# Performance work log

Measured on AMD Instinct MI355X. Metric: run time of the kernel, lower is better.

## Reference

```python
import jax, jax.numpy as jnp
import numpy as np

ALPHA = 0.2  # LeakyReLU negative slope
MASK_FILL = -9e15


def setup_inputs() -> dict:
    key = jax.random.key(0)
    k_x, k_adj, k_W, k_a = jax.random.split(key, 4)
    B, N, Fin, T, O = 8, 1024, 64, 8, 128
    x = jax.random.normal(k_x, (B, N, Fin, T), dtype=jnp.float32)
    adj = (jax.random.uniform(k_adj, (N, N)) < 0.05).astype(jnp.float32)
    adj = jnp.maximum(adj, jnp.eye(N, dtype=jnp.float32))
    W = jax.random.normal(k_W, (Fin, O), dtype=jnp.float32) * (1.414 * (6.0 / (Fin + O)) ** 0.5)
    a = jax.random.normal(k_a, (2 * O, 1), dtype=jnp.float32) * (1.414 * (6.0 / (2 * O + 1)) ** 0.5)
    return {"x": x, "adj": adj, "W": W, "a": a}


def reference(x, adj, W, a):
    # x: (B, N, Fin, T), adj: (N, N), W: (Fin, O), a: (2O, 1)
    O = W.shape[1]
    xt = jnp.transpose(x, (0, 3, 1, 2))                 # (B, T, N, Fin)
    Wh = jnp.einsum('btnf,fo->btno', xt, W)             # (B, T, N, O)
    a1 = a[:O, 0]                                       # (O,)
    a2 = a[O:, 0]                                       # (O,)
    Wh1 = Wh @ a1                                       # (B, T, N)
    Wh2 = Wh @ a2                                       # (B, T, N)
    e = Wh1[..., :, None] + Wh2[..., None, :]           # (B, T, N, N): e_ij = Wh1_i + Wh2_j
    e = jax.nn.leaky_relu(e, negative_slope=ALPHA)
    e = jnp.where(adj > 0, e, MASK_FILL)
    attn = jax.nn.softmax(e, axis=-1)                   # softmax over neighbors j (torch dim=1 on (N,N))
    # dropout on attention is identity at inference (training=False)
    h_prime = jnp.einsum('btij,btjo->btio', attn, Wh)   # (B, T, N, O)
    out = jnp.transpose(h_prime, (0, 2, 3, 1))          # (B, N, O, T)
    return jax.nn.elu(out)                              # concat=True -> ELU
```

## Files before the change

kernel.cpp:

```cpp
#include <hip/hip_runtime.h>
#include <math.h>
#include <stdint.h>

#define ALPHA 0.2f

typedef __attribute__((ext_vector_type(8)))  short bf16x8;
typedef __attribute__((ext_vector_type(4)))  float f32x4;
typedef __attribute__((ext_vector_type(16))) float f32x16;

__device__ __forceinline__ uint32_t pack_bf16(float a, float b) {
    return ((__float_as_uint(a) + 0x8000u) >> 16) |
           ((__float_as_uint(b) + 0x8000u) & 0xFFFF0000u);
}

__global__ __launch_bounds__(512) void k_wh(const float* __restrict__ x,
                                            const float* __restrict__ W,
                                            const float* __restrict__ a,
                                            uint4* __restrict__ Whf,
                                            float* __restrict__ Wh1,
                                            float* __restrict__ Wh2) {
    __shared__ float xs[16 * 512];
    __shared__ float Wv[128 * 68];

    const int tid = threadIdx.x;
    const int b   = blockIdx.x & 7;
    const int jt  = blockIdx.x >> 3;

    const float4* xg4 = (const float4*)(x + (size_t)(b * 1024 + jt * 16) * 512);
    #pragma unroll
    for (int i = 0; i < 4; ++i) {
        int    idx = tid + i * 512;
        float4 v   = xg4[idx];
        int jl  = idx >> 7;
        int rem = idx & 127;
        int f   = rem >> 1;
        int tq  = rem & 1;
        int kk  = f ^ ((jl >> 2) << 2);
        float* dst = &xs[jl * 512 + (tq * 4) * 64 + kk];
        dst[0]   = v.x;
        dst[64]  = v.y;
        dst[128] = v.z;
        dst[192] = v.w;
    }
    const float4* Wg4 = (const float4*)W;
    #pragma unroll
    for (int i = 0; i < 4; ++i) {
        int    idx = tid + i * 512;
        float4 v   = Wg4[idx];
        int k  = idx >> 5;
        int o0 = (idx & 31) * 4;
        #pragma unroll
        for (int c = 0; c < 4; ++c) {
            int o   = o0 + c;
            int adr = o * 68 + ((((k >> 2) ^ ((o >> 3) & 7)) << 2) | (k & 3));
            Wv[adr] = (&v.x)[c];
        }
    }
    __syncthreads();

    const int w  = tid >> 6;
    const int l  = tid & 63;
    const int q  = l >> 4;
    const int om = l & 15;
    const int t  = w;

    float acc[4][8];
    #pragma unroll
    for (int jj = 0; jj < 4; ++jj)
        #pragma unroll
        for (int nt = 0; nt < 8; ++nt) acc[jj][nt] = 0.f;

    for (int kc = 0; kc < 64; kc += 4) {
        float4 xv[4], wv[8];
        const int kx = kc ^ (q << 2);
        #pragma unroll
        for (int jj = 0; jj < 4; ++jj)
            xv[jj] = *(const float4*)&xs[(q * 4 + jj) * 512 + t * 64 + kx];
        #pragma unroll
        for (int nt = 0; nt < 8; ++nt) {
            int og  = nt * 16 + om;
            int grp = (kc >> 2) ^ ((nt * 2 + (om >> 3)) & 7);
            wv[nt]  = *(const float4*)&Wv[og * 68 + grp * 4];
        }
        #pragma unroll
        for (int jj = 0; jj < 4; ++jj) {
            #pragma unroll
            for (int nt = 0; nt < 8; ++nt) {
                float s = acc[jj][nt];
                s = fmaf(xv[jj].x, wv[nt].x, s);
                s = fmaf(xv[jj].y, wv[nt].y, s);
                s = fmaf(xv[jj].z, wv[nt].z, s);
                s = fmaf(xv[jj].w, wv[nt].w, s);
                acc[jj][nt] = s;
            }
        }
    }

    const int bt = b * 8 + t;

    float a1v[8], a2v[8];
    #pragma unroll
    for (int nt = 0; nt < 8; ++nt) {
        a1v[nt] = a[nt * 16 + om];
        a2v[nt] = a[128 + nt * 16 + om];
    }
    #pragma unroll
    for (int jj = 0; jj < 4; ++jj) {
        float s1 = 0.f, s2 = 0.f;
        #pragma unroll
        for (int nt = 0; nt < 8; ++nt) {
            s1 = fmaf(acc[jj][nt], a1v[nt], s1);
            s2 = fmaf(acc[jj][nt], a2v[nt], s2);
        }
        #pragma unroll
        for (int off = 1; off < 16; off <<= 1) {
            s1 += __shfl_xor(s1, off);
            s2 += __shfl_xor(s2, off);
        }
        if (om == 0) {
            int j = jt * 16 + q * 4 + jj;
            Wh1[bt * 1024 + j] = s1;
            Wh2[bt * 1024 + j] = s2;
        }
    }

    #pragma unroll
    for (int nt = 0; nt < 8; ++nt) {
        uint2 st;
        st.x = pack_bf16(acc[0][nt], acc[1][nt]);
        st.y = pack_bf16(acc[2][nt], acc[3][nt]);
        int    lane2 = ((q >> 1) << 5) | ((nt & 1) << 4) | om;
        size_t fidx  = ((size_t)(bt * 4 + (nt >> 1)) * 64 + jt) * 64 + lane2;
        char*  p     = (char*)(Whf + fidx) + ((q & 1) << 3);
        *(uint2*)p = st;
    }
}

__global__ __launch_bounds__(256) void k_adjb(const float* __restrict__ adj,
                                              unsigned char* __restrict__ adjq) {
    int idx = blockIdx.x * 256 + threadIdx.x;
    int i   = idx >> 7;
    int pos = idx & 127;
    const float4* a4 = (const float4*)adj + idx * 2;
    float4 v0 = a4[0], v1 = a4[1];
    unsigned int by = 0;
    by |= (v0.x > 0.f) ? 1u : 0u;
    by |= (v0.y > 0.f) ? 2u : 0u;
    by |= (v0.z > 0.f) ? 4u : 0u;
    by |= (v0.w > 0.f) ? 8u : 0u;
    by |= (v1.x > 0.f) ? 16u : 0u;
    by |= (v1.y > 0.f) ? 32u : 0u;
    by |= (v1.z > 0.f) ? 64u : 0u;
    by |= (v1.w > 0.f) ? 128u : 0u;
    adjq[(i << 7) + ((pos & 1) << 6) + (((pos >> 1) & 1) << 5) + (pos >> 2)] = (unsigned char)by;
}

__global__ __launch_bounds__(256) void k_agg(const uint4* __restrict__ Whf,
                                             const float* __restrict__ Wh1,
                                             const float* __restrict__ Wh2,
                                             const unsigned char* __restrict__ adjq,
                                             float* __restrict__ out) {
    __shared__ __attribute__((aligned(16))) uint4    bstage[2][1024];
    __shared__ __attribute__((aligned(16))) uint32_t efs[1024];
    __shared__ float wh1s[128];
    __shared__ float m2s[4];

    const int tid   = threadIdx.x;
    const int b     = blockIdx.x & 7;
    const int t     = (blockIdx.x >> 3) & 7;
    const int itile = blockIdx.x >> 6;
    const int bt    = b * 8 + t;
    const int i0    = itile * 128;

    const int w   = tid >> 6;
    const int l   = tid & 63;
    const int col = l & 31;
    const int g   = l >> 5;
    const int row = w * 32 + col;

    const uint4* plane = Whf + (size_t)bt * 16384;
    const int    c     = w;
    const int    li    = l;

    uint4 pf[4];
    #pragma unroll
    for (int f = 0; f < 4; ++f) pf[f] = plane[(c * 64 + f) * 64 + li];

    const uint4* ap = (const uint4*)(adjq + ((size_t)(i0 + row) << 7) + (g << 6));
    uint4 am[4];
    #pragma unroll
    for (int f = 0; f < 4; ++f) am[f] = ap[f];

    const float* wh2g = Wh2 + bt * 1024;
    float mx = -1e30f;
    #pragma unroll
    for (int rep = 0; rep < 4; ++rep) {
        int   j  = tid + rep * 256;
        float h2 = wh2g[j];
        float E  = __expf(h2);
        float F  = __expf(ALPHA * h2);
        efs[j] = pack_bf16(E, F);
        mx = fmaxf(mx, h2);
    }
    #pragma unroll
    for (int off = 1; off < 64; off <<= 1) mx = fmaxf(mx, __shfl_xor(mx, off));
    if (l == 0) m2s[w] = mx;
    if (tid < 128) wh1s[tid] = Wh1[bt * 1024 + i0 + tid];

    #pragma unroll
    for (int f = 0; f < 4; ++f) bstage[0][(c * 4 + f) * 64 + li] = pf[f];
    __syncthreads();

    const float M2 = fmaxf(fmaxf(m2s[0], m2s[1]), fmaxf(m2s[2], m2s[3]));
    const float h1 = wh1s[row];
    const float e0 = h1 + M2;
    const float mp = fmaxf(e0, ALPHA * e0);
    const float Af = __expf(h1 - mp);
    const float Bf = __expf(ALPHA * h1 - mp);
    const float G  = __expf(-h1);

    f32x16 acc[4];
    #pragma unroll
    for (int nt2 = 0; nt2 < 4; ++nt2)
        #pragma unroll
        for (int r = 0; r < 16; ++r) acc[nt2][r] = 0.f;
    f32x16 accl;
    #pragma unroll
    for (int r = 0; r < 16; ++r) accl[r] = 0.f;

    bf16x8 ones;
    #pragma unroll
    for (int i = 0; i < 8; ++i) ones[i] = (short)0x3F80;

    #pragma unroll
    for (int u = 0; u < 16; ++u) {
        if (u + 1 < 16) {
            #pragma unroll
            for (int f = 0; f < 4; ++f)
                pf[f] = plane[(c * 64 + (u + 1) * 4 + f) * 64 + li];
        }

        #pragma unroll
        for (int d = 0; d < 2; ++d) {
            const int s = u * 2 + d;
            #pragma unroll
            for (int h = 0; h < 2; ++h) {
                const int jb = s * 32 + h * 16 + g * 8;
                uint4 efa = *(const uint4*)&efs[jb];
                uint4 efb = *(const uint4*)&efs[jb + 4];
                uint32_t ef[8] = {efa.x, efa.y, efa.z, efa.w,
                                  efb.x, efb.y, efb.z, efb.w};

                const int      pe = h * 32 + s;
                const uint4    av = am[pe >> 4];
                const int      cc = (pe >> 2) & 3;
                const uint32_t cw = (cc == 0) ? av.x : (cc == 1) ? av.y
                                   : (cc == 2) ? av.z : av.w;
                const uint32_t by = (cw >> ((pe & 3) * 8)) & 0xFFu;

                float p[8];
                #pragma unroll
                for (int e = 0; e < 8; ++e) {
                    float E  = __uint_as_float(ef[e] << 16);
                    float F  = __uint_as_float(ef[e] & 0xFFFF0000u);
                    bool  cd = E > G;
                    float pr = (cd ? Af : Bf) * (cd ? E : F);
                    p[e] = ((by >> e) & 1u) ? pr : 0.0f;
                }
                union { uint32_t u32[4]; bf16x8 v; } pk;
                #pragma unroll
                for (int r = 0; r < 4; ++r)
                    pk.u32[r] = pack_bf16(p[2 * r], p[2 * r + 1]);

                #pragma unroll
                for (int nt2 = 0; nt2 < 4; ++nt2) {
                    union { uint4 u4; bf16x8 v; } br;
                    br.u4 = bstage[u & 1][(nt2 * 4 + d * 2 + h) * 64 + l];
                    acc[nt2] = __builtin_amdgcn_mfma_f32_32x32x16_bf16(
                        pk.v, br.v, acc[nt2], 0, 0, 0);
                }
                accl = __builtin_amdgcn_mfma_f32_32x32x16_bf16(
                    pk.v, ones, accl, 0, 0, 0);
            }
        }

        if (u + 1 < 16) {
            #pragma unroll
            for (int f = 0; f < 4; ++f)
                bstage[(u + 1) & 1][(c * 4 + f) * 64 + li] = pf[f];
        }
        __syncthreads();
    }

    float* og = out + ((size_t)(b * 1024 + i0 + w * 32)) * 1024 + t;
    #pragma unroll
    for (int reg = 0; reg < 16; ++reg) {
        const int   r    = (reg & 3) + 8 * (reg >> 2) + 4 * g;
        const float linv = 1.0f / accl[reg];
        #pragma unroll
        for (int nt2 = 0; nt2 < 4; ++nt2) {
            float v = acc[nt2][reg] * linv;
            v = v > 0.f ? v : __expf(v) - 1.f;
            og[(size_t)r * 1024 + (nt2 * 32 + col) * 8] = v;
        }
    }
}

extern "C" void kernel_launch(void* const* d_in, const int* in_sizes, int n_in,
                              void* d_out, int out_size, void* d_ws, size_t ws_size,
                              hipStream_t stream) {
    const float* x   = (const float*)d_in[0];
    const float* adj = (const float*)d_in[1];
    const float* W   = (const float*)d_in[2];
    const float* a   = (const float*)d_in[3];
    float* out = (float*)d_out;

    uint4*         Whf  = (uint4*)d_ws;
    float*         Wh1  = (float*)(Whf + 1048576);
    float*         Wh2  = Wh1 + 65536;
    unsigned char* adjq = (unsigned char*)(Wh2 + 65536);

    k_wh  <<<512, 512, 0, stream>>>(x, W, a, Whf, Wh1, Wh2);
    k_adjb<<<512, 256, 0, stream>>>(adj, adjq);
    k_agg <<<512, 256, 0, stream>>>(Whf, Wh1, Wh2, adjq, out);
}
```

Measured before the change: 150.4 us.

## Double stage size, use fp32 exp tables and fmax-based leaky-softmax weights

The aggregation loop now runs 8 stages of 128 neighbors instead of 16 stages of 64, which halves the number of block barriers and makes each prefetch larger. E and F exponentials are stored as separate fp32 tables, so the bf16 unpacking goes away. The branchy select is replaced by fmax of the two scaled exponentials, with a multiply by the adjacency bit. In exchange, LDS use roughly doubles for staging, more prefetch registers are live, and each neighbor now needs four LDS vector loads instead of two.

```diff
diff --git a/kernel.cpp b/kernel.cpp
--- a/kernel.cpp
+++ b/kernel.cpp
@@ -160,8 +160,9 @@
                                              const float* __restrict__ Wh2,
                                              const unsigned char* __restrict__ adjq,
                                              float* __restrict__ out) {
-    __shared__ __attribute__((aligned(16))) uint4    bstage[2][1024];
-    __shared__ __attribute__((aligned(16))) uint32_t efs[1024];
+    __shared__ __attribute__((aligned(16))) uint4 bstage[2][2048];
+    __shared__ __attribute__((aligned(16))) float efsE[1024];
+    __shared__ __attribute__((aligned(16))) float efsF[1024];
     __shared__ float wh1s[128];
     __shared__ float m2s[4];
 
@@ -179,12 +180,10 @@
     const int row = w * 32 + col;
 
     const uint4* plane = Whf + (size_t)bt * 16384;
-    const int    c     = w;
-    const int    li    = l;
-
-    uint4 pf[4];
-    #pragma unroll
-    for (int f = 0; f < 4; ++f) pf[f] = plane[(c * 64 + f) * 64 + li];
+
+    uint4 pf[8];
+    #pragma unroll
+    for (int f = 0; f < 8; ++f) pf[f] = plane[(w * 64 + f) * 64 + l];
 
     const uint4* ap = (const uint4*)(adjq + ((size_t)(i0 + row) << 7) + (g << 6));
     uint4 am[4];
@@ -197,9 +196,8 @@
     for (int rep = 0; rep < 4; ++rep) {
         int   j  = tid + rep * 256;
         float h2 = wh2g[j];
-        float E  = __expf(h2);
-        float F  = __expf(ALPHA * h2);
-        efs[j] = pack_bf16(E, F);
+        efsE[j] = __expf(h2);
+        efsF[j] = __expf(ALPHA * h2);
         mx = fmaxf(mx, h2);
     }
     #pragma unroll
@@ -208,7 +206,7 @@
     if (tid < 128) wh1s[tid] = Wh1[bt * 1024 + i0 + tid];
 
     #pragma unroll
-    for (int f = 0; f < 4; ++f) bstage[0][(c * 4 + f) * 64 + li] = pf[f];
+    for (int f = 0; f < 8; ++f) bstage[0][(w * 8 + f) * 64 + l] = pf[f];
     __syncthreads();
 
     const float M2 = fmaxf(fmaxf(m2s[0], m2s[1]), fmaxf(m2s[2], m2s[3]));
@@ -217,7 +215,6 @@
     const float mp = fmaxf(e0, ALPHA * e0);
     const float Af = __expf(h1 - mp);
     const float Bf = __expf(ALPHA * h1 - mp);
-    const float G  = __expf(-h1);
 
     f32x16 acc[4];
     #pragma unroll
@@ -233,61 +230,58 @@
     for (int i = 0; i < 8; ++i) ones[i] = (short)0x3F80;
 
     #pragma unroll
-    for (int u = 0; u < 16; ++u) {
-        if (u + 1 < 16) {
-            #pragma unroll
-            for (int f = 0; f < 4; ++f)
-                pf[f] = plane[(c * 64 + (u + 1) * 4 + f) * 64 + li];
-        }
-
-        #pragma unroll
-        for (int d = 0; d < 2; ++d) {
-            const int s = u * 2 + d;
-            #pragma unroll
-            for (int h = 0; h < 2; ++h) {
-                const int jb = s * 32 + h * 16 + g * 8;
-                uint4 efa = *(const uint4*)&efs[jb];
-                uint4 efb = *(const uint4*)&efs[jb + 4];
-                uint32_t ef[8] = {efa.x, efa.y, efa.z, efa.w,
-                                  efb.x, efb.y, efb.z, efb.w};
-
-                const int      pe = h * 32 + s;
-                const uint4    av = am[pe >> 4];
-                const int      cc = (pe >> 2) & 3;
-                const uint32_t cw = (cc == 0) ? av.x : (cc == 1) ? av.y
-                                   : (cc == 2) ? av.z : av.w;
-                const uint32_t by = (cw >> ((pe & 3) * 8)) & 0xFFu;
-
-                float p[8];
-                #pragma unroll
-                for (int e = 0; e < 8; ++e) {
-                    float E  = __uint_as_float(ef[e] << 16);
-                    float F  = __uint_as_float(ef[e] & 0xFFFF0000u);
-                    bool  cd = E > G;
-                    float pr = (cd ? Af : Bf) * (cd ? E : F);
-                    p[e] = ((by >> e) & 1u) ? pr : 0.0f;
-                }
-                union { uint32_t u32[4]; bf16x8 v; } pk;
-                #pragma unroll
-                for (int r = 0; r < 4; ++r)
-                    pk.u32[r] = pack_bf16(p[2 * r], p[2 * r + 1]);
-
-                #pragma unroll
-                for (int nt2 = 0; nt2 < 4; ++nt2) {
-                    union { uint4 u4; bf16x8 v; } br;
-                    br.u4 = bstage[u & 1][(nt2 * 4 + d * 2 + h) * 64 + l];
-                    acc[nt2] = __builtin_amdgcn_mfma_f32_32x32x16_bf16(
-                        pk.v, br.v, acc[nt2], 0, 0, 0);
-                }
-                accl = __builtin_amdgcn_mfma_f32_32x32x16_bf16(
-                    pk.v, ones, accl, 0, 0, 0);
+    for (int u = 0; u < 8; ++u) {
+        if (u + 1 < 8) {
+            #pragma unroll
+            for (int f = 0; f < 8; ++f)
+                pf[f] = plane[(w * 64 + (u + 1) * 8 + f) * 64 + l];
+        }
+
+        #pragma unroll
+        for (int ts = 0; ts < 8; ++ts) {
+            const int jb = u * 128 + ts * 16 + g * 8;
+            float4 E0 = *(const float4*)&efsE[jb];
+            float4 E1 = *(const float4*)&efsE[jb + 4];
+            float4 F0 = *(const float4*)&efsF[jb];
+            float4 F1 = *(const float4*)&efsF[jb + 4];
+
+            const int      pe = (ts & 1) * 32 + u * 4 + (ts >> 1);
+            const uint4    av = am[pe >> 4];
+            const int      cc = (pe >> 2) & 3;
+            const uint32_t cw = (cc == 0) ? av.x : (cc == 1) ? av.y
+                               : (cc == 2) ? av.z : av.w;
+            const uint32_t by = (cw >> ((pe & 3) * 8)) & 0xFFu;
+
+            float p[8];
+            p[0] = fmaxf(Af * E0.x, Bf * F0.x) * (float)((by >> 0) & 1u);
+            p[1] = fmaxf(Af * E0.y, Bf * F0.y) * (float)((by >> 1) & 1u);
+            p[2] = fmaxf(Af * E0.z, Bf * F0.z) * (float)((by >> 2) & 1u);
+            p[3] = fmaxf(Af * E0.w, Bf * F0.w) * (float)((by >> 3) & 1u);
+            p[4] = fmaxf(Af * E1.x, Bf * F1.x) * (float)((by >> 4) & 1u);
+            p[5] = fmaxf(Af * E1.y, Bf * F1.y) * (float)((by >> 5) & 1u);
+            p[6] = fmaxf(Af * E1.z, Bf * F1.z) * (float)((by >> 6) & 1u);
+            p[7] = fmaxf(Af * E1.w, Bf * F1.w) * (float)((by >> 7) & 1u);
+
+            union { uint32_t u32[4]; bf16x8 v; } pk;
+            #pragma unroll
+            for (int r = 0; r < 4; ++r)
+                pk.u32[r] = pack_bf16(p[2 * r], p[2 * r + 1]);
+
+            #pragma unroll
+            for (int nt2 = 0; nt2 < 4; ++nt2) {
+                union { uint4 u4; bf16x8 v; } br;
+                br.u4 = bstage[u & 1][(nt2 * 8 + ts) * 64 + l];
+                acc[nt2] = __builtin_amdgcn_mfma_f32_32x32x16_bf16(
+                    pk.v, br.v, acc[nt2], 0, 0, 0);
             }
-        }
-
-        if (u + 1 < 16) {
-            #pragma unroll
-            for (int f = 0; f < 4; ++f)
-                bstage[(u + 1) & 1][(c * 4 + f) * 64 + li] = pf[f];
+            accl = __builtin_amdgcn_mfma_f32_32x32x16_bf16(
+                pk.v, ones, accl, 0, 0, 0);
+        }
+
+        if (u + 1 < 8) {
+            #pragma unroll
+            for (int f = 0; f < 8; ++f)
+                bstage[(u + 1) & 1][(w * 8 + f) * 64 + l] = pf[f];
         }
         __syncthreads();
     }
```

Result: faster. 143.8 us (-4.4%).
